# Kernel optimization log

Hardware: AMD Instinct MI355X
Metric: run time of the kernel (lower is better)

Reference implementation:

```python
import jax, jax.numpy as jnp
import numpy as np

NUM_ITEMS = 50000
EMBED = 256
HEADS = 8
HEAD_DIM = EMBED // HEADS
B, S = 32, 512
NEG_BIG = -1e9   # mask fill for dot-product scores
NEG_SMALL = -1e5 # mask fill for rel / time maps (as in RKT)


def setup_inputs() -> dict:
    key = jax.random.key(0)
    ks = jax.random.split(key, 20)
    sc = 0.02
    return {
        "item_inputs": jax.random.randint(ks[0], (B, S), 0, NUM_ITEMS + 1),
        "label_inputs": jax.random.randint(ks[1], (B, S), 0, 2, dtype=jnp.int32),
        "item_ids": jax.random.randint(ks[2], (B, S), 0, NUM_ITEMS + 1),
        "rel": jax.random.uniform(ks[3], (B, S, S), jnp.float32),
        "timestamp": jax.random.uniform(ks[4], (B, S, S), jnp.float32) * 10.0,
        # learned params
        "item_embeds": jax.random.normal(ks[5], (NUM_ITEMS + 1, EMBED), jnp.float32) * sc,
        "W_in": jax.random.normal(ks[6], (2 * EMBED, EMBED), jnp.float32) * sc,
        "b_in": jnp.zeros((EMBED,), jnp.float32),
        "Wq": jax.random.normal(ks[7], (EMBED, EMBED), jnp.float32) * sc,
        "bq": jnp.zeros((EMBED,), jnp.float32),
        "Wk": jax.random.normal(ks[8], (EMBED, EMBED), jnp.float32) * sc,
        "bk": jnp.zeros((EMBED,), jnp.float32),
        "Wv": jax.random.normal(ks[9], (EMBED, EMBED), jnp.float32) * sc,
        "bv": jnp.zeros((EMBED,), jnp.float32),
        "W_out": jax.random.normal(ks[10], (EMBED, 1), jnp.float32) * sc,
        "b_out": jnp.zeros((1,), jnp.float32),
        "l1": jnp.float32(0.5),
        "l2": jnp.float32(0.5),
    }


def _split_heads(t, W, b):
    # [B,S,E] -> [B,H,S,HD]
    return (t @ W + b).reshape(B, S, HEADS, HEAD_DIM).transpose(0, 2, 1, 3)


def reference(item_inputs, label_inputs, item_ids, rel, timestamp, item_embeds,
              W_in, b_in, Wq, bq, Wk, bk, Wv, bv, W_out, b_out, l1, l2):
    # --- input construction: response-gated duplicated item embedding ---
    e = item_embeds[item_inputs]                       # [B,S,E]
    lab = label_inputs[..., None].astype(e.dtype)      # [B,S,1]
    inputs = jnp.concatenate([e * lab, e * (1.0 - lab)], axis=-1)  # [B,S,2E]
    inputs = jax.nn.relu(inputs @ W_in + b_in)         # [B,S,E]
    query = item_embeds[item_ids]                      # [B,S,E]

    future = jnp.triu(jnp.ones((S, S), bool), 1)       # True above diagonal

    Q = _split_heads(query, Wq, bq)
    K = _split_heads(inputs, Wk, bk)
    V = _split_heads(inputs, Wv, bv)

    # scaled dot-product scores with causal mask
    scores = jnp.einsum('bhqd,bhkd->bhqk', Q, K) / np.float32(np.sqrt(HEAD_DIM))
    prob_attn = jax.nn.softmax(jnp.where(future, NEG_BIG, scores), axis=-1)

    # relational (item-item correlation) attention, future-masked
    rel_m = rel * (~future).astype(rel.dtype)          # [B,S,S]
    rel_attn = jax.nn.softmax(jnp.where(rel_m == 0, NEG_SMALL, rel_m), axis=-1)
    rel_attn = rel_attn[:, None]                       # broadcast over heads

    # exponential time-decay attention, future-masked
    ts = jnp.exp(-jnp.abs(timestamp))
    time_attn = jax.nn.softmax(jnp.where(future, NEG_SMALL, ts), axis=-1)[:, None]

    attn = (1.0 - l2) * prob_attn + l2 * time_attn
    attn = (1.0 - l1) * attn + l1 * rel_attn           # [B,H,S,S]

    out = jnp.einsum('bhqk,bhkd->bhqd', attn, V)       # [B,H,S,HD]
    out = out.transpose(0, 2, 1, 3).reshape(B, S, EMBED)
    logits = out @ W_out + b_out                       # [B,S,1]
    return logits, attn
```

## Files before the change

### kernel.cpp

```cpp
#include <hip/hip_runtime.h>
#include <hip/hip_bf16.h>

#define SEQ 512
#define EMB 256
#define NHEAD 8
#define HD 32

using bf16x8 = __attribute__((ext_vector_type(8))) short;
using f32x4  = __attribute__((ext_vector_type(4))) float;

static __device__ __forceinline__ unsigned short f2bf(float x) {
    union { float f; unsigned int u; } v; v.f = x;
    unsigned int r = v.u + 0x7FFFu + ((v.u >> 16) & 1u);
    return (unsigned short)(r >> 16);
}
static __device__ __forceinline__ float bf2f(unsigned short v) {
    union { unsigned int u; float f; } w; w.u = ((unsigned int)v) << 16; return w.f;
}

__global__ __launch_bounds__(256) void fused_prep_kernel(
    const int* __restrict__ item_inputs,
    const int* __restrict__ label_inputs,
    const int* __restrict__ item_ids,
    const float* __restrict__ embeds,
    const float* __restrict__ W_in,
    const float* __restrict__ Wq,
    const float* __restrict__ Wk,
    const float* __restrict__ Wv,
    const float* __restrict__ Wout,
    const float* __restrict__ bv,
    const float* __restrict__ bout,
    const float* __restrict__ rel,
    const float* __restrict__ tsp,
    unsigned short* __restrict__ Abig,
    unsigned short* __restrict__ qbf,
    unsigned short* __restrict__ WTin,
    unsigned short* __restrict__ WTq,
    unsigned short* __restrict__ WTk,
    float* __restrict__ Wvw,
    float* __restrict__ bvw,
    float* __restrict__ logits,
    float* __restrict__ dent,
    float* __restrict__ denr)
{
    const int bid = blockIdx.x;
    const int t = threadIdx.x;

    if (bid < 4096) {
        int r = bid * 4 + (t >> 6);
        int j = (t & 63) * 4;
        int item = item_inputs[r];
        int lab  = label_inputs[r];
        int qid  = item_ids[r];
        float4 e4 = *(const float4*)(embeds + (size_t)item * EMB + j);
        ushort4 on  = make_ushort4(f2bf(e4.x), f2bf(e4.y), f2bf(e4.z), f2bf(e4.w));
        ushort4 off = make_ushort4(0, 0, 0, 0);
        *(ushort4*)(Abig + (size_t)r * 512 + j)       = lab ? on : off;
        *(ushort4*)(Abig + (size_t)r * 512 + 256 + j) = lab ? off : on;
        float4 q4 = *(const float4*)(embeds + (size_t)qid * EMB + j);
        *(ushort4*)(qbf + (size_t)r * 256 + j) =
            make_ushort4(f2bf(q4.x), f2bf(q4.y), f2bf(q4.z), f2bf(q4.w));
    } else if (bid < 5193) {
        int idx = (bid - 4096) * 256 + t;
        if (idx < 131072) {
            int n = idx >> 9, k = idx & 511;
            WTin[idx] = f2bf(W_in[(size_t)k * 256 + n]);
        } else if (idx < 196608) {
            int i = idx - 131072;
            int n = i >> 8, k = i & 255;
            WTq[i] = f2bf(Wq[(size_t)k * 256 + n]);
        } else if (idx < 262144) {
            int i = idx - 196608;
            int n = i >> 8, k = i & 255;
            WTk[i] = f2bf(Wk[(size_t)k * 256 + n]);
        } else if (idx < 264192) {
            int i = idx - 262144;
            int c = i >> 3, h = i & 7;
            float s = 0.f;
            #pragma unroll
            for (int d = 0; d < 32; d++)
                s += Wv[(size_t)c * 256 + h * 32 + d] * Wout[h * 32 + d];
            Wvw[i] = s;
        } else if (idx < 264200) {
            int h = idx - 264192;
            float s = 0.f;
            #pragma unroll
            for (int d = 0; d < 32; d++) s += bv[h * 32 + d] * Wout[h * 32 + d];
            bvw[h] = s;
        } else if (idx < 280584) {
            logits[idx - 264200] = bout[0];
        }
    } else {
        const int id2 = bid - 5193;
        const int b = id2 >> 4;
        const int qt = id2 & 15;
        const int q0 = qt * 32;
        const int row = t >> 3;
        const int lane8 = t & 7;
        const int qrow = q0 + row;
        const size_t base = ((size_t)(b * SEQ) + qrow) * SEQ;
        float dt = 0.f, dr = 0.f;
        for (int k4 = lane8 * 4; k4 <= qrow; k4 += 32) {
            float4 tv4 = *(const float4*)(tsp + base + k4);
            float4 rv4 = *(const float4*)(rel + base + k4);
            const float* tvp = &tv4.x;
            const float* rvp = &rv4.x;
            #pragma unroll
            for (int j = 0; j < 4; j++) {
                const bool va = (k4 + j) <= qrow;
                dt += va ? __expf(__expf(-fabsf(tvp[j]))) : 0.f;
                dr += (va && rvp[j] != 0.f) ? __expf(rvp[j]) : 0.f;
            }
        }
        dt += __shfl_xor(dt, 1); dt += __shfl_xor(dt, 2); dt += __shfl_xor(dt, 4);
        dr += __shfl_xor(dr, 1); dr += __shfl_xor(dr, 2); dr += __shfl_xor(dr, 4);
        if (lane8 == 0) {
            dent[b * SEQ + qrow] = dt;
            denr[b * SEQ + qrow] = dr;
        }
    }
}

template<int KDIM, int RELU, int OUTBF>
static __device__ __forceinline__ void gemm_body(
    const unsigned short* __restrict__ A,
    const unsigned short* __restrict__ BT,
    const float* __restrict__ bias,
    void* __restrict__ Cout, float scale)
{
    __shared__ unsigned short As[64][40];
    __shared__ unsigned short Bs[128][40];
    const int t = threadIdx.x;
    const int row0 = blockIdx.x * 64;
    const int col0 = blockIdx.y * 128;
    const int wid = t >> 6, lane = t & 63;
    const int wm = wid & 1, wn = wid >> 1;
    const int lg = lane >> 4, l15 = lane & 15;

    f32x4 acc[2][4];
    #pragma unroll
    for (int i = 0; i < 2; i++)
        #pragma unroll
        for (int j = 0; j < 4; j++) acc[i][j] = (f32x4){0.f, 0.f, 0.f, 0.f};

    const int arow = t >> 2, achk = t & 3;
    const int brow = t >> 1, bhalf = t & 1;

    for (int k0 = 0; k0 < KDIM; k0 += 32) {
        __syncthreads();
        *(uint4*)(&As[arow][achk * 8]) =
            *(const uint4*)(A + (size_t)(row0 + arow) * KDIM + k0 + achk * 8);
        const unsigned short* bsrc = BT + (size_t)(col0 + brow) * KDIM + k0 + bhalf * 16;
        *(uint4*)(&Bs[brow][bhalf * 16])     = *(const uint4*)(bsrc);
        *(uint4*)(&Bs[brow][bhalf * 16 + 8]) = *(const uint4*)(bsrc + 8);
        __syncthreads();
        bf16x8 af[2], bfr[4];
        #pragma unroll
        for (int fm = 0; fm < 2; fm++)
            af[fm] = *(const bf16x8*)(&As[wm * 32 + fm * 16 + l15][lg * 8]);
        #pragma unroll
        for (int fn = 0; fn < 4; fn++)
            bfr[fn] = *(const bf16x8*)(&Bs[wn * 64 + fn * 16 + l15][lg * 8]);
        #pragma unroll
        for (int fm = 0; fm < 2; fm++)
            #pragma unroll
            for (int fn = 0; fn < 4; fn++)
                acc[fm][fn] = __builtin_amdgcn_mfma_f32_16x16x32_bf16(
                    af[fm], bfr[fn], acc[fm][fn], 0, 0, 0);
    }
    #pragma unroll
    for (int fm = 0; fm < 2; fm++)
        #pragma unroll
        for (int fn = 0; fn < 4; fn++) {
            int col = col0 + wn * 64 + fn * 16 + l15;
            float bvv = bias[col];
            #pragma unroll
            for (int r = 0; r < 4; r++) {
                int row = row0 + wm * 32 + fm * 16 + lg * 4 + r;
                float v = acc[fm][fn][r] + bvv;
                if (RELU) v = fmaxf(v, 0.f);
                v *= scale;
                if (OUTBF) ((unsigned short*)Cout)[(size_t)row * 256 + col] = f2bf(v);
                else       ((float*)Cout)[(size_t)row * 256 + col] = v;
            }
        }
}

__global__ __launch_bounds__(256, 2) void gemmA_kernel(
    const unsigned short* __restrict__ Abig,
    const unsigned short* __restrict__ WTin,
    const float* __restrict__ b_in,
    unsigned short* __restrict__ Xbf,
    const unsigned short* __restrict__ qbf,
    const unsigned short* __restrict__ WTq,
    const float* __restrict__ bq,
    unsigned short* __restrict__ Qbf)
{
    if (blockIdx.z == 0)
        gemm_body<512, 1, 1>(Abig, WTin, b_in, (void*)Xbf, 1.0f);
    else
        gemm_body<256, 0, 1>(qbf, WTq, bq, (void*)Qbf, 0.17677669529663687f);
}

static __device__ __forceinline__ void vw_body(
    const unsigned short* __restrict__ Xbf,
    const float* __restrict__ Wvw,
    const float* __restrict__ bvw,
    float* __restrict__ Vw)
{
    __shared__ float sW[2048];
    __shared__ float sb[8];
    int t = threadIdx.x;
    #pragma unroll
    for (int i = 0; i < 8; i++) sW[i * 256 + t] = Wvw[i * 256 + t];
    if (t < 8) sb[t] = bvw[t];
    __syncthreads();
    int row = blockIdx.x * 256 + t;
    float acc[8];
    #pragma unroll
    for (int h = 0; h < 8; h++) acc[h] = sb[h];
    for (int d0 = 0; d0 < 32; d0++) {
        bf16x8 x = *(const bf16x8*)(Xbf + (size_t)row * 256 + d0 * 8);
        #pragma unroll
        for (int j = 0; j < 8; j++) {
            float xf = bf2f((unsigned short)x[j]);
            #pragma unroll
            for (int h = 0; h < 8; h++) acc[h] += xf * sW[(d0 * 8 + j) * 8 + h];
        }
    }
    *(float4*)(Vw + (size_t)row * 8)     = make_float4(acc[0], acc[1], acc[2], acc[3]);
    *(float4*)(Vw + (size_t)row * 8 + 4) = make_float4(acc[4], acc[5], acc[6], acc[7]);
}

__global__ __launch_bounds__(256, 2) void gemmB_kernel(
    const unsigned short* __restrict__ Xbf,
    const unsigned short* __restrict__ WTk,
    const float* __restrict__ bk,
    unsigned short* __restrict__ Kbf,
    const float* __restrict__ Wvw,
    const float* __restrict__ bvw,
    float* __restrict__ Vw)
{
    if (blockIdx.z == 0) {
        gemm_body<256, 0, 1>(Xbf, WTk, bk, (void*)Kbf, 1.0f);
    } else {
        if (blockIdx.x >= 64 || blockIdx.y != 0) return;
        vw_body(Xbf, Wvw, bvw, Vw);
    }
}

__global__ __launch_bounds__(256, 4) void attnW_kernel(
    const unsigned short* __restrict__ Qbf,
    const unsigned short* __restrict__ Kbf,
    const float* __restrict__ Vw,
    const float* __restrict__ rel,
    const float* __restrict__ tsp,
    const float* __restrict__ dent,
    const float* __restrict__ denr,
    const float* __restrict__ pl1,
    const float* __restrict__ pl2,
    float* __restrict__ logits,
    float* __restrict__ attn)
{
    __shared__ float sP[16][516];
    __shared__ float sVw[512];
    __shared__ float sden[4][16];

    const int t = threadIdx.x;
    const int id = blockIdx.x;
    const int qt16 = 31 - (id >> 8);
    const int b = (id >> 3) & 31;
    const int h = id & 7;
    const int q0 = qt16 * 16;
    const int qmax = q0 + 15;

    const int w = t >> 6, lane = t & 63;
    const int l15 = lane & 15, lg = lane >> 4;

    const float l1 = pl1[0], l2 = pl2[0];
    const float cp = (1.f - l1) * (1.f - l2);
    const float ct = (1.f - l1) * l2;
    const float cr = l1;

    sVw[t]       = Vw[((size_t)(b * SEQ) + t) * 8 + h];
    sVw[256 + t] = Vw[((size_t)(b * SEQ) + 256 + t) * 8 + h];

    bf16x8 aq = *(const bf16x8*)(Qbf + (size_t)(b * SEQ + q0 + l15) * EMB + h * 32 + lg * 8);

    float dp[4] = {0.f, 0.f, 0.f, 0.f};
    #pragma unroll
    for (int ki = 0; ki < 4; ki++) {
        const int kt = w + ki * 4;
        const int k0 = kt * 32;
        if (k0 <= qmax) {
            #pragma unroll
            for (int nf = 0; nf < 2; nf++) {
                const int kcol = k0 + nf * 16 + l15;
                const int lcol = k0 + nf * 16 + l15;
                bf16x8 bk = *(const bf16x8*)(Kbf +
                    (size_t)(b * SEQ + kcol) * EMB + h * 32 + lg * 8);
                f32x4 am = __builtin_amdgcn_mfma_f32_16x16x32_bf16(
                    aq, bk, (f32x4){0.f, 0.f, 0.f, 0.f}, 0, 0, 0);
                #pragma unroll
                for (int r = 0; r < 4; r++) {
                    const int qloc = lg * 4 + r;
                    float e = (kcol <= q0 + qloc) ? __expf(am[r]) : 0.f;
                    sP[qloc][lcol] = e;
                    dp[r] += e;
                }
            }
        } else {
            #pragma unroll
            for (int nf = 0; nf < 2; nf++)
                #pragma unroll
                for (int r = 0; r < 4; r++)
                    sP[lg * 4 + r][k0 + nf * 16 + l15] = 0.f;
        }
    }
    #pragma unroll
    for (int r = 0; r < 4; r++) {
        float v = dp[r];
        v += __shfl_xor(v, 1); v += __shfl_xor(v, 2);
        v += __shfl_xor(v, 4); v += __shfl_xor(v, 8);
        if (l15 == 0) sden[w][lg * 4 + r] = v;
    }
    __syncthreads();

    const int wrow = t >> 4;
    const int wcol = (t & 15) * 4;
    const int qrow_w = q0 + wrow;
    const float den = sden[0][wrow] + sden[1][wrow] + sden[2][wrow] + sden[3][wrow];
    const float cpinv = cp / den;
    const float dtv = dent[b * SEQ + qrow_w];
    const float drv = denr[b * SEQ + qrow_w];
    const float ctt = ct / dtv;
    const float crr = drv > 0.f ? cr / drv : 0.f;

    float* arow = attn + ((size_t)((b * NHEAD + h) * SEQ) + qrow_w) * SEQ;
    const size_t rbase = ((size_t)(b * SEQ) + qrow_w) * SEQ;
    const f32x4 z4 = (f32x4){0.f, 0.f, 0.f, 0.f};
    float plog = 0.f;

    #pragma unroll
    for (int s = 0; s < 8; s++) {
        const int c = wcol + s * 64;
        f32x4 o;
        if (c > qrow_w) {
            o = z4;
        } else {
            float4 tv4 = *(const float4*)(tsp + rbase + c);
            float4 rv4 = *(const float4*)(rel + rbase + c);
            const float* tvp = &tv4.x;
            const float* rvp = &rv4.x;
            #pragma unroll
            for (int j = 0; j < 4; j++) {
                const bool va = (c + j) <= qrow_w;
                float e_t = va ? __expf(__expf(-fabsf(tvp[j]))) * ctt : 0.f;
                float e_r = (va && rvp[j] != 0.f) ? __expf(rvp[j]) * crr : 0.f;
                float a = fmaf(sP[wrow][c + j], cpinv, e_t + e_r);
                a = va ? a : 0.f;
                o[j] = a;
                plog = fmaf(a, sVw[c + j], plog);
            }
        }
        __builtin_nontemporal_store(o, (f32x4*)(arow + c));
    }

    plog += __shfl_xor(plog, 1); plog += __shfl_xor(plog, 2);
    plog += __shfl_xor(plog, 4); plog += __shfl_xor(plog, 8);
    if ((t & 15) == 0)
        atomicAdd(&logits[b * SEQ + qrow_w], plog);
}

extern "C" void kernel_launch(void* const* d_in, const int* in_sizes, int n_in,
                              void* d_out, int out_size, void* d_ws, size_t ws_size,
                              hipStream_t stream)
{
    (void)in_sizes; (void)n_in; (void)out_size; (void)ws_size;
    const int*   item_inputs  = (const int*)d_in[0];
    const int*   label_inputs = (const int*)d_in[1];
    const int*   item_ids     = (const int*)d_in[2];
    const float* rel   = (const float*)d_in[3];
    const float* tsp   = (const float*)d_in[4];
    const float* emb   = (const float*)d_in[5];
    const float* W_in  = (const float*)d_in[6];
    const float* b_in  = (const float*)d_in[7];
    const float* Wq    = (const float*)d_in[8];
    const float* bq    = (const float*)d_in[9];
    const float* Wk    = (const float*)d_in[10];
    const float* bk    = (const float*)d_in[11];
    const float* Wv    = (const float*)d_in[12];
    const float* bv    = (const float*)d_in[13];
    const float* Wout  = (const float*)d_in[14];
    const float* bout  = (const float*)d_in[15];
    const float* l1    = (const float*)d_in[16];
    const float* l2    = (const float*)d_in[17];

    const size_t R = 16384;
    char* w = (char*)d_ws;
    unsigned short* Abig = (unsigned short*)w; w += R * 512 * 2;
    unsigned short* qbf  = (unsigned short*)w; w += R * 256 * 2;
    unsigned short* WTin = (unsigned short*)w; w += (size_t)256 * 512 * 2;
    unsigned short* WTq  = (unsigned short*)w; w += (size_t)256 * 256 * 2;
    unsigned short* WTk  = (unsigned short*)w; w += (size_t)256 * 256 * 2;
    unsigned short* Xbf  = (unsigned short*)w; w += R * 256 * 2;
    unsigned short* Qbf  = (unsigned short*)w; w += R * 256 * 2;
    unsigned short* Kbf  = (unsigned short*)w; w += R * 256 * 2;
    float* Wvw  = (float*)w; w += 2048 * 4;
    float* Vw   = (float*)w; w += R * 8 * 4;
    float* bvw  = (float*)w; w += 256;
    float* dent = (float*)w; w += (size_t)32 * SEQ * 4;
    float* denr = (float*)w; w += (size_t)32 * SEQ * 4;

    float* logits = (float*)d_out;
    float* attnp  = (float*)d_out + 16384;

    fused_prep_kernel<<<dim3(5705), dim3(256), 0, stream>>>(
        item_inputs, label_inputs, item_ids, emb,
        W_in, Wq, Wk, Wv, Wout, bv, bout, rel, tsp,
        Abig, qbf, WTin, WTq, WTk, Wvw, bvw, logits, dent, denr);

    gemmA_kernel<<<dim3(256, 2, 2), dim3(256), 0, stream>>>(
        Abig, WTin, b_in, Xbf, qbf, WTq, bq, Qbf);

    gemmB_kernel<<<dim3(256, 2, 2), dim3(256), 0, stream>>>(
        Xbf, WTk, bk, Kbf, Wvw, bvw, Vw);

    attnW_kernel<<<dim3(8192), dim3(256), 0, stream>>>(
        Qbf, Kbf, Vw, rel, tsp, dent, denr, l1, l2, logits, attnp);
}
```

Before: 153.7 us.

## Store attention probs as bf16 in LDS and rebalance denominator prep blocks

The attention kernel now keeps the exponentiated scores in shared memory as bf16 instead of fp32, halving LDS use so the launch bound can ask for 8 blocks per CU instead of 4. In the prep kernel the rel/time denominator blocks move to the front of the grid, use 16 lanes per row with 16-row tiles, and are ordered longest-first so the heavy rows start early. The bf16 rounding of the probabilities lowers precision of the prob_attn term in the output attention, and the higher occupancy target may limit registers per thread.

Result: faster. 145.2 us (median of 2 runs) (-5.5%).

```diff
diff --git a/kernel.cpp b/kernel.cpp
--- a/kernel.cpp
+++ b/kernel.cpp
@@ -46,8 +46,37 @@
     const int bid = blockIdx.x;
     const int t = threadIdx.x;
 
-    if (bid < 4096) {
-        int r = bid * 4 + (t >> 6);
+    if (bid < 1024) {
+        const int b = bid >> 5;
+        const int s16 = 31 - (bid & 31);
+        const int q0 = s16 * 16;
+        const int row = t >> 4;
+        const int lane16 = t & 15;
+        const int qrow = q0 + row;
+        const size_t base = ((size_t)(b * SEQ) + qrow) * SEQ;
+        float dt = 0.f, dr = 0.f;
+        for (int k4 = lane16 * 4; k4 <= qrow; k4 += 64) {
+            float4 tv4 = *(const float4*)(tsp + base + k4);
+            float4 rv4 = *(const float4*)(rel + base + k4);
+            const float* tvp = &tv4.x;
+            const float* rvp = &rv4.x;
+            #pragma unroll
+            for (int j = 0; j < 4; j++) {
+                const bool va = (k4 + j) <= qrow;
+                dt += va ? __expf(__expf(-fabsf(tvp[j]))) : 0.f;
+                dr += (va && rvp[j] != 0.f) ? __expf(rvp[j]) : 0.f;
+            }
+        }
+        dt += __shfl_xor(dt, 1); dt += __shfl_xor(dt, 2);
+        dt += __shfl_xor(dt, 4); dt += __shfl_xor(dt, 8);
+        dr += __shfl_xor(dr, 1); dr += __shfl_xor(dr, 2);
+        dr += __shfl_xor(dr, 4); dr += __shfl_xor(dr, 8);
+        if (lane16 == 0) {
+            dent[b * SEQ + qrow] = dt;
+            denr[b * SEQ + qrow] = dr;
+        }
+    } else if (bid < 5120) {
+        int r = (bid - 1024) * 4 + (t >> 6);
         int j = (t & 63) * 4;
         int item = item_inputs[r];
         int lab  = label_inputs[r];
@@ -60,8 +89,8 @@
         float4 q4 = *(const float4*)(embeds + (size_t)qid * EMB + j);
         *(ushort4*)(qbf + (size_t)r * 256 + j) =
             make_ushort4(f2bf(q4.x), f2bf(q4.y), f2bf(q4.z), f2bf(q4.w));
-    } else if (bid < 5193) {
-        int idx = (bid - 4096) * 256 + t;
+    } else {
+        int idx = (bid - 5120) * 256 + t;
         if (idx < 131072) {
             int n = idx >> 9, k = idx & 511;
             WTin[idx] = f2bf(W_in[(size_t)k * 256 + n]);
@@ -90,34 +119,6 @@
         } else if (idx < 280584) {
             logits[idx - 264200] = bout[0];
         }
-    } else {
-        const int id2 = bid - 5193;
-        const int b = id2 >> 4;
-        const int qt = id2 & 15;
-        const int q0 = qt * 32;
-        const int row = t >> 3;
-        const int lane8 = t & 7;
-        const int qrow = q0 + row;
-        const size_t base = ((size_t)(b * SEQ) + qrow) * SEQ;
-        float dt = 0.f, dr = 0.f;
-        for (int k4 = lane8 * 4; k4 <= qrow; k4 += 32) {
-            float4 tv4 = *(const float4*)(tsp + base + k4);
-            float4 rv4 = *(const float4*)(rel + base + k4);
-            const float* tvp = &tv4.x;
-            const float* rvp = &rv4.x;
-            #pragma unroll
-            for (int j = 0; j < 4; j++) {
-                const bool va = (k4 + j) <= qrow;
-                dt += va ? __expf(__expf(-fabsf(tvp[j]))) : 0.f;
-                dr += (va && rvp[j] != 0.f) ? __expf(rvp[j]) : 0.f;
-            }
-        }
-        dt += __shfl_xor(dt, 1); dt += __shfl_xor(dt, 2); dt += __shfl_xor(dt, 4);
-        dr += __shfl_xor(dr, 1); dr += __shfl_xor(dr, 2); dr += __shfl_xor(dr, 4);
-        if (lane8 == 0) {
-            dent[b * SEQ + qrow] = dt;
-            denr[b * SEQ + qrow] = dr;
-        }
     }
 }
 
@@ -249,7 +250,7 @@
     }
 }
 
-__global__ __launch_bounds__(256, 4) void attnW_kernel(
+__global__ __launch_bounds__(256, 8) void attnW_kernel(
     const unsigned short* __restrict__ Qbf,
     const unsigned short* __restrict__ Kbf,
     const float* __restrict__ Vw,
@@ -262,7 +263,7 @@
     float* __restrict__ logits,
     float* __restrict__ attn)
 {
-    __shared__ float sP[16][516];
+    __shared__ unsigned short sP[16][520];
     __shared__ float sVw[512];
     __shared__ float sden[4][16];
 
@@ -296,7 +297,6 @@
             #pragma unroll
             for (int nf = 0; nf < 2; nf++) {
                 const int kcol = k0 + nf * 16 + l15;
-                const int lcol = k0 + nf * 16 + l15;
                 bf16x8 bk = *(const bf16x8*)(Kbf +
                     (size_t)(b * SEQ + kcol) * EMB + h * 32 + lg * 8);
                 f32x4 am = __builtin_amdgcn_mfma_f32_16x16x32_bf16(
@@ -305,7 +305,7 @@
                 for (int r = 0; r < 4; r++) {
                     const int qloc = lg * 4 + r;
                     float e = (kcol <= q0 + qloc) ? __expf(am[r]) : 0.f;
-                    sP[qloc][lcol] = e;
+                    sP[qloc][kcol] = f2bf(e);
                     dp[r] += e;
                 }
             }
@@ -314,7 +314,7 @@
             for (int nf = 0; nf < 2; nf++)
                 #pragma unroll
                 for (int r = 0; r < 4; r++)
-                    sP[lg * 4 + r][k0 + nf * 16 + l15] = 0.f;
+                    sP[lg * 4 + r][k0 + nf * 16 + l15] = 0;
         }
     }
     #pragma unroll
@@ -350,14 +350,16 @@
         } else {
             float4 tv4 = *(const float4*)(tsp + rbase + c);
             float4 rv4 = *(const float4*)(rel + rbase + c);
+            ushort4 p4 = *(const ushort4*)(&sP[wrow][c]);
             const float* tvp = &tv4.x;
             const float* rvp = &rv4.x;
+            const unsigned short* pp = &p4.x;
             #pragma unroll
             for (int j = 0; j < 4; j++) {
                 const bool va = (c + j) <= qrow_w;
                 float e_t = va ? __expf(__expf(-fabsf(tvp[j]))) * ctt : 0.f;
                 float e_r = (va && rvp[j] != 0.f) ? __expf(rvp[j]) * crr : 0.f;
-                float a = fmaf(sP[wrow][c + j], cpinv, e_t + e_r);
+                float a = fmaf(bf2f(pp[j]), cpinv, e_t + e_r);
                 a = va ? a : 0.f;
                 o[j] = a;
                 plog = fmaf(a, sVw[c + j], plog);
@@ -415,7 +417,7 @@
     float* logits = (float*)d_out;
     float* attnp  = (float*)d_out + 16384;
 
-    fused_prep_kernel<<<dim3(5705), dim3(256), 0, stream>>>(
+    fused_prep_kernel<<<dim3(6217), dim3(256), 0, stream>>>(
         item_inputs, label_inputs, item_ids, emb,
         W_in, Wq, Wk, Wv, Wout, bv, bout, rel, tsp,
         Abig, qbf, WTin, WTq, WTk, Wvw, bvw, logits, dent, denr);
```
